# Kernel tuning notes

Hardware: AMD Instinct MI355X
Metric: run time of the kernel (lower is better)

The kernel has to match this reference:

```python
import jax, jax.numpy as jnp
import numpy as np

STATE_DIM = 32
CONTROL_DIM = 8
EMBED_DIM = 96
LATENT_DIM = STATE_DIM + EMBED_DIM  # 128
HIDDEN = 512
B, M = 2048, 64


def setup_inputs() -> dict:
    key = jax.random.key(0)
    ks = jax.random.split(key, 16)
    s = lambda k, shp, fan: jax.random.normal(k, shp, jnp.float32) * (1.0 / np.sqrt(fan))
    return {
        "x_k": jax.random.normal(ks[0], (B, STATE_DIM), jnp.float32),
        "u_seq": jax.random.normal(ks[1], (B, M, CONTROL_DIM), jnp.float32),
        "x_next_seq": jax.random.normal(ks[2], (B, M, STATE_DIM), jnp.float32),
        # encoder MLP (depth=3): in->h, h->h, h->h, h->embed
        "W1": s(ks[3], (STATE_DIM, HIDDEN), STATE_DIM), "b1": jnp.zeros((HIDDEN,), jnp.float32),
        "W2": s(ks[4], (HIDDEN, HIDDEN), HIDDEN), "b2": jnp.zeros((HIDDEN,), jnp.float32),
        "W3": s(ks[5], (HIDDEN, HIDDEN), HIDDEN), "b3": jnp.zeros((HIDDEN,), jnp.float32),
        "Wo": s(ks[6], (HIDDEN, EMBED_DIM), HIDDEN), "bo": jnp.zeros((EMBED_DIM,), jnp.float32),
        # Koopman operators (Linear, no bias); stored as [in, out]
        "A": s(ks[7], (LATENT_DIM, LATENT_DIM), LATENT_DIM),
        "Bmat": s(ks[8], (CONTROL_DIM, LATENT_DIM), CONTROL_DIM),
    }


def _encode(x, W1, b1, W2, b2, W3, b3, Wo, bo):
    h = jax.nn.relu(x @ W1 + b1)
    h = jax.nn.relu(h @ W2 + b2)
    h = jax.nn.relu(h @ W3 + b3)
    return h @ Wo + bo


def _lift(x, W1, b1, W2, b2, W3, b3, Wo, bo):
    return jnp.concatenate([x, _encode(x, W1, b1, W2, b2, W3, b3, Wo, bo)], axis=-1)


def reference(x_k, u_seq, x_next_seq, W1, b1, W2, b2, W3, b3, Wo, bo, A, Bmat):
    m = u_seq.shape[1]
    z_k = _lift(x_k, W1, b1, W2, b2, W3, b3, Wo, bo)  # [B, L]
    # lift targets (encoder applied to flattened [B*M, S])
    z_target_seq = _lift(x_next_seq.reshape(-1, STATE_DIM), W1, b1, W2, b2, W3, b3, Wo, bo)
    z_target_seq = z_target_seq.reshape(-1, m, LATENT_DIM)
    # precompute control contributions, then sequential LTI recurrence via scan
    bu = jnp.einsum('bmc,cl->mbl', u_seq, Bmat)  # [M, B, L]

    def step(z, bu_i):
        z_next = z @ A + bu_i
        return z_next, z_next

    _, z_pred = jax.lax.scan(step, z_k, bu)  # [M, B, L]
    z_pred_seq = jnp.transpose(z_pred, (1, 0, 2))  # [B, M, L]
    x_pred_seq = z_pred_seq[..., :STATE_DIM]
    return (z_pred_seq, x_pred_seq, z_target_seq)
```

## Files before the change

kernel.cpp:

```cpp
#include <hip/hip_runtime.h>


typedef unsigned short u16;
typedef __attribute__((ext_vector_type(8))) short bf16x8;
typedef __attribute__((ext_vector_type(4))) short bf16x4;
typedef __attribute__((ext_vector_type(4))) float f32x4;

#define OFF_W1 0
#define OFF_W2 16384
#define OFF_W3 278528
#define OFF_WO 540672
#define OFF_ZK_BYTES 1179648

#define XPRED_OFF 16777216
#define ZTGT_OFF  20971520

__device__ __forceinline__ float bf2f(u16 u) {
  unsigned int i = ((unsigned int)u) << 16;
  return __builtin_bit_cast(float, i);
}
__device__ __forceinline__ u16 f2bf(float f) {
  unsigned int i = __builtin_bit_cast(unsigned int, f);
  i = (i + 0x7FFFu + ((i >> 16) & 1u)) >> 16;
  return (u16)i;
}

__global__ void prep_swizzle(const float* __restrict__ W1, const float* __restrict__ W2,
                             const float* __restrict__ W3, const float* __restrict__ Wo,
                             u16* __restrict__ dst) {
  int f = blockIdx.x;
  int l = threadIdx.x;
  const float* src; int K, N; u16* d;
  if (f < 32)        { src = W1; K = 32;  N = 512; d = dst + OFF_W1; }
  else if (f < 544)  { src = W2; K = 512; N = 512; d = dst + OFF_W2; f -= 32; }
  else if (f < 1056) { src = W3; K = 512; N = 512; d = dst + OFF_W3; f -= 544; }
  else               { src = Wo; K = 512; N = 96;  d = dst + OFF_WO; f -= 1056; }
  const int KF = K >> 5;
  const int ct = f / KF, ks = f - ct * KF;
  const int q = l >> 4, n = l & 15;
  const int kbase = ks * 32 + q * 8;
  const int col = ct * 16 + n;
  bf16x8 vh;
  #pragma unroll
  for (int j = 0; j < 8; ++j)
    vh[j] = (short)f2bf(src[(size_t)(kbase + j) * N + col]);
  *(bf16x8*)(d + ((size_t)f * 64 + l) * 8) = vh;
}

__device__ __forceinline__ void store_h(const f32x4 (&acc)[4][4],
                                        const float* __restrict__ bias,
                                        u16* hbuf, int wv, int q, int n) {
  __syncthreads();
  #pragma unroll
  for (int i = 0; i < 4; ++i) {
    const int col = wv * 64 + i * 16 + n;
    const float bia = bias[col];
    #pragma unroll
    for (int rg = 0; rg < 4; ++rg) {
      #pragma unroll
      for (int r = 0; r < 4; ++r) {
        const int row = rg * 16 + q * 4 + r;
        hbuf[(row * 512 + col) ^ ((row & 7) << 3)] = f2bf(fmaxf(acc[rg][i][r] + bia, 0.f));
      }
    }
  }
  __syncthreads();
}

__device__ __forceinline__ void big_layer(const u16* __restrict__ wb,
                                          const float* __restrict__ bias,
                                          u16* hbuf, int wv, int l, int q, int n) {
  f32x4 acc[4][4];
  #pragma unroll
  for (int rg = 0; rg < 4; ++rg)
    #pragma unroll
    for (int i = 0; i < 4; ++i) acc[rg][i] = (f32x4){0.f, 0.f, 0.f, 0.f};
  #pragma unroll 2
  for (int ks = 0; ks < 16; ++ks) {
    bf16x8 b[4], a[4];
    #pragma unroll
    for (int i = 0; i < 4; ++i)
      b[i] = *(const bf16x8*)(wb + (size_t)((4 * wv + i) * 16 + ks) * 512 + (size_t)l * 8);
    #pragma unroll
    for (int rg = 0; rg < 4; ++rg) {
      const int row = rg * 16 + n;
      a[rg] = *(const bf16x8*)&hbuf[(row * 512 + ks * 32 + q * 8) ^ ((row & 7) << 3)];
    }
    #pragma unroll
    for (int rg = 0; rg < 4; ++rg)
      #pragma unroll
      for (int i = 0; i < 4; ++i)
        acc[rg][i] = __builtin_amdgcn_mfma_f32_16x16x32_bf16(a[rg], b[i], acc[rg][i], 0, 0, 0);
  }
  store_h(acc, bias, hbuf, wv, q, n);
}

__global__ __launch_bounds__(512, 2) void encoder_tgt(
    const float* __restrict__ xnext, const u16* __restrict__ wf,
    const float* __restrict__ b1, const float* __restrict__ b2,
    const float* __restrict__ b3, const float* __restrict__ bo_,
    float* __restrict__ ztgt) {
  __shared__ __align__(16) u16 hbuf[64 * 512];
  const int tid = threadIdx.x;
  const int wv = tid >> 6, l = tid & 63;
  const int q = l >> 4, n = l & 15;
  const size_t row0 = (size_t)blockIdx.x * 64;

  {
    const int r = tid >> 3, k0 = (tid & 7) * 4;
    f32x4 x = *(const f32x4*)(xnext + (row0 + r) * 32 + k0);
    *(f32x4*)(ztgt + (row0 + r) * 128 + k0) = x;
    bf16x4 v;
    #pragma unroll
    for (int j = 0; j < 4; ++j) v[j] = (short)f2bf(x[j]);
    *(bf16x4*)&hbuf[(r * 512 + k0) ^ ((r & 7) << 3)] = v;
  }
  __syncthreads();

  {
    f32x4 acc[4][4];
    #pragma unroll
    for (int rg = 0; rg < 4; ++rg)
      #pragma unroll
      for (int i = 0; i < 4; ++i) acc[rg][i] = (f32x4){0.f, 0.f, 0.f, 0.f};
    bf16x8 a[4];
    #pragma unroll
    for (int rg = 0; rg < 4; ++rg) {
      const int row = rg * 16 + n;
      a[rg] = *(const bf16x8*)&hbuf[(row * 512 + q * 8) ^ ((row & 7) << 3)];
    }
    #pragma unroll
    for (int i = 0; i < 4; ++i) {
      bf16x8 b = *(const bf16x8*)(wf + OFF_W1 + (size_t)(4 * wv + i) * 512 + (size_t)l * 8);
      #pragma unroll
      for (int rg = 0; rg < 4; ++rg)
        acc[rg][i] = __builtin_amdgcn_mfma_f32_16x16x32_bf16(a[rg], b, acc[rg][i], 0, 0, 0);
    }
    store_h(acc, b1, hbuf, wv, q, n);
  }

  big_layer(wf + OFF_W2, b2, hbuf, wv, l, q, n);
  big_layer(wf + OFF_W3, b3, hbuf, wv, l, q, n);

  if (wv < 6) {
    f32x4 o[4];
    #pragma unroll
    for (int rg = 0; rg < 4; ++rg) o[rg] = (f32x4){0.f, 0.f, 0.f, 0.f};
    #pragma unroll 2
    for (int ks = 0; ks < 16; ++ks) {
      bf16x8 b = *(const bf16x8*)(wf + OFF_WO + (size_t)(wv * 16 + ks) * 512 + (size_t)l * 8);
      #pragma unroll
      for (int rg = 0; rg < 4; ++rg) {
        const int row = rg * 16 + n;
        bf16x8 a = *(const bf16x8*)&hbuf[(row * 512 + ks * 32 + q * 8) ^ ((row & 7) << 3)];
        o[rg] = __builtin_amdgcn_mfma_f32_16x16x32_bf16(a, b, o[rg], 0, 0, 0);
      }
    }
    const float bia = bo_[wv * 16 + n];
    #pragma unroll
    for (int rg = 0; rg < 4; ++rg)
      #pragma unroll
      for (int r = 0; r < 4; ++r)
        ztgt[(row0 + rg * 16 + q * 4 + r) * 128 + 32 + wv * 16 + n] = o[rg][r] + bia;
  }
}

__global__ __launch_bounds__(256) void encoder_zk_f32(
    const float* __restrict__ xk,
    const float* __restrict__ W1, const float* __restrict__ b1,
    const float* __restrict__ W2, const float* __restrict__ b2,
    const float* __restrict__ W3, const float* __restrict__ b3,
    const float* __restrict__ Wo, const float* __restrict__ bo_,
    float* __restrict__ zk_out) {
  __shared__ __align__(16) float hb[2][8][512];
  __shared__ __align__(16) float xb[8][32];
  const int t = threadIdx.x;
  const int row0 = blockIdx.x * 8;
  {
    int r = t >> 5, j = t & 31;
    float v = xk[(size_t)(row0 + r) * 32 + j];
    xb[r][j] = v;
    zk_out[(size_t)(row0 + r) * 128 + j] = v;
  }
  __syncthreads();
  const int c0 = t, c1 = t + 256;
  {
    float a0[8], a1[8];
    const float i0 = b1[c0], i1 = b1[c1];
    #pragma unroll
    for (int r = 0; r < 8; ++r) { a0[r] = i0; a1[r] = i1; }
    for (int k = 0; k < 32; k += 4) {
      float w00 = W1[(size_t)(k+0)*512 + c0], w10 = W1[(size_t)(k+0)*512 + c1];
      float w01 = W1[(size_t)(k+1)*512 + c0], w11 = W1[(size_t)(k+1)*512 + c1];
      float w02 = W1[(size_t)(k+2)*512 + c0], w12 = W1[(size_t)(k+2)*512 + c1];
      float w03 = W1[(size_t)(k+3)*512 + c0], w13 = W1[(size_t)(k+3)*512 + c1];
      #pragma unroll
      for (int r = 0; r < 8; ++r) {
        f32x4 z = *(const f32x4*)&xb[r][k];
        a0[r] += z[0]*w00 + z[1]*w01 + z[2]*w02 + z[3]*w03;
        a1[r] += z[0]*w10 + z[1]*w11 + z[2]*w12 + z[3]*w13;
      }
    }
    #pragma unroll
    for (int r = 0; r < 8; ++r) { hb[0][r][c0] = fmaxf(a0[r], 0.f); hb[0][r][c1] = fmaxf(a1[r], 0.f); }
  }
  __syncthreads();
  #pragma unroll
  for (int lyr = 0; lyr < 2; ++lyr) {
    const float* W = lyr ? W3 : W2;
    const float* bb = lyr ? b3 : b2;
    const float (*hin)[512] = hb[lyr & 1];
    float (*hout)[512] = hb[(lyr & 1) ^ 1];
    float a0[8], a1[8];
    const float i0 = bb[c0], i1 = bb[c1];
    #pragma unroll
    for (int r = 0; r < 8; ++r) { a0[r] = i0; a1[r] = i1; }
    for (int k = 0; k < 512; k += 4) {
      float w00 = W[(size_t)(k+0)*512 + c0], w10 = W[(size_t)(k+0)*512 + c1];
      float w01 = W[(size_t)(k+1)*512 + c0], w11 = W[(size_t)(k+1)*512 + c1];
      float w02 = W[(size_t)(k+2)*512 + c0], w12 = W[(size_t)(k+2)*512 + c1];
      float w03 = W[(size_t)(k+3)*512 + c0], w13 = W[(size_t)(k+3)*512 + c1];
      #pragma unroll
      for (int r = 0; r < 8; ++r) {
        f32x4 z = *(const f32x4*)&hin[r][k];
        a0[r] += z[0]*w00 + z[1]*w01 + z[2]*w02 + z[3]*w03;
        a1[r] += z[0]*w10 + z[1]*w11 + z[2]*w12 + z[3]*w13;
      }
    }
    #pragma unroll
    for (int r = 0; r < 8; ++r) { hout[r][c0] = fmaxf(a0[r], 0.f); hout[r][c1] = fmaxf(a1[r], 0.f); }
    __syncthreads();
  }
  if (t < 96) {
    float a[8];
    const float i0 = bo_[t];
    #pragma unroll
    for (int r = 0; r < 8; ++r) a[r] = i0;
    for (int k = 0; k < 512; k += 4) {
      float w0 = Wo[(size_t)(k+0)*96 + t];
      float w1 = Wo[(size_t)(k+1)*96 + t];
      float w2 = Wo[(size_t)(k+2)*96 + t];
      float w3 = Wo[(size_t)(k+3)*96 + t];
      #pragma unroll
      for (int r = 0; r < 8; ++r) {
        f32x4 z = *(const f32x4*)&hb[0][r][k];
        a[r] += z[0]*w0 + z[1]*w1 + z[2]*w2 + z[3]*w3;
      }
    }
    #pragma unroll
    for (int r = 0; r < 8; ++r)
      zk_out[(size_t)(row0 + r) * 128 + 32 + t] = a[r];
  }
}

__global__ __launch_bounds__(256, 2) void scan_kernel(
    const float* __restrict__ zk, const float* __restrict__ Af,
    const float* __restrict__ Bm, const float* __restrict__ useq,
    float* __restrict__ zpred, float* __restrict__ xpred) {
  __shared__ __align__(16) float ubuf[4 * 512];
  __shared__ __align__(16) float zbuf[2][4 * 128];
  const int t = threadIdx.x;
  const int b0 = blockIdx.x * 4;
  const int c = t & 127, g = t >> 7;

  *(f32x4*)&ubuf[t * 4]        = *(const f32x4*)(useq + (size_t)b0 * 512 + t * 4);
  *(f32x4*)&ubuf[1024 + t * 4] = *(const f32x4*)(useq + (size_t)b0 * 512 + 1024 + t * 4);
  if (t < 128) *(f32x4*)&zbuf[0][t * 4] = *(const f32x4*)(zk + (size_t)b0 * 128 + t * 4);

  f32x4 ar[32];
  #pragma unroll
  for (int kk = 0; kk < 32; ++kk) {
    ar[kk][0] = Af[(size_t)(4 * kk + 0) * 128 + c];
    ar[kk][1] = Af[(size_t)(4 * kk + 1) * 128 + c];
    ar[kk][2] = Af[(size_t)(4 * kk + 2) * 128 + c];
    ar[kk][3] = Af[(size_t)(4 * kk + 3) * 128 + c];
  }
  float bm[8];
  #pragma unroll
  for (int j = 0; j < 8; ++j) bm[j] = Bm[j * 128 + c];
  __syncthreads();

  const int r0 = 2 * g, r1 = 2 * g + 1;
  const size_t o0 = (size_t)(b0 + r0) * 64;
  const size_t o1 = (size_t)(b0 + r1) * 64;
  int cur = 0;
  #pragma unroll 1
  for (int s = 0; s < 64; ++s) {
    f32x4 ua0 = *(const f32x4*)&ubuf[r0 * 512 + s * 8];
    f32x4 ub0 = *(const f32x4*)&ubuf[r0 * 512 + s * 8 + 4];
    f32x4 ua1 = *(const f32x4*)&ubuf[r1 * 512 + s * 8];
    f32x4 ub1 = *(const f32x4*)&ubuf[r1 * 512 + s * 8 + 4];
    f32x4 v0, v1;
    #pragma unroll
    for (int j = 0; j < 4; ++j) {
      v0[j] = ua0[j] * bm[j] + ub0[j] * bm[4 + j];
      v1[j] = ua1[j] * bm[j] + ub1[j] * bm[4 + j];
    }
    const float* z0p = &zbuf[cur][r0 * 128];
    const float* z1p = &zbuf[cur][r1 * 128];
    #pragma unroll
    for (int kk = 0; kk < 32; ++kk) {
      f32x4 a  = ar[kk];
      f32x4 za = *(const f32x4*)&z0p[kk * 4];
      f32x4 zb = *(const f32x4*)&z1p[kk * 4];
      v0 += za * a;
      v1 += zb * a;
    }
    const float acc0 = (v0[0] + v0[1]) + (v0[2] + v0[3]);
    const float acc1 = (v1[0] + v1[1]) + (v1[2] + v1[3]);
    zbuf[cur ^ 1][r0 * 128 + c] = acc0;
    zbuf[cur ^ 1][r1 * 128 + c] = acc1;
    zpred[(o0 + s) * 128 + c] = acc0;
    zpred[(o1 + s) * 128 + c] = acc1;
    if (c < 32) {
      xpred[(o0 + s) * 32 + c] = acc0;
      xpred[(o1 + s) * 32 + c] = acc1;
    }
    __syncthreads();
    cur ^= 1;
  }
}

extern "C" void kernel_launch(void* const* d_in, const int* in_sizes, int n_in,
                              void* d_out, int out_size, void* d_ws, size_t ws_size,
                              hipStream_t stream) {
  (void)in_sizes; (void)n_in; (void)out_size; (void)ws_size;
  const float* xk    = (const float*)d_in[0];
  const float* useq  = (const float*)d_in[1];
  const float* xnext = (const float*)d_in[2];
  const float* W1 = (const float*)d_in[3];
  const float* b1 = (const float*)d_in[4];
  const float* W2 = (const float*)d_in[5];
  const float* b2 = (const float*)d_in[6];
  const float* W3 = (const float*)d_in[7];
  const float* b3 = (const float*)d_in[8];
  const float* Wo = (const float*)d_in[9];
  const float* bo = (const float*)d_in[10];
  const float* A  = (const float*)d_in[11];
  const float* Bm = (const float*)d_in[12];

  float* out   = (float*)d_out;
  float* zpred = out;
  float* xpred = out + XPRED_OFF;
  float* ztgt  = out + ZTGT_OFF;
  u16*   wf    = (u16*)d_ws;
  float* zkw   = (float*)((char*)d_ws + OFF_ZK_BYTES);

  prep_swizzle<<<1152, 64, 0, stream>>>(W1, W2, W3, Wo, wf);
  encoder_zk_f32<<<256, 256, 0, stream>>>(xk, W1, b1, W2, b2, W3, b3, Wo, bo, zkw);
  scan_kernel<<<512, 256, 0, stream>>>(zkw, A, Bm, useq, zpred, xpred);
  encoder_tgt<<<2048, 512, 0, stream>>>(xnext, wf, b1, b2, b3, bo, ztgt);
}
```

Baseline: 528.7 us.

## Move Koopman scan to split-bf16 MFMA and widen encoder blocks

The scan recurrence now runs on bf16 MFMA with a hi/lo split of both A and z (three MFMAs per tile) to approximate fp32 accuracy. A is pre-split by the prep kernel and loaded into LDS with global_load_lds, and each block handles 8 batch rows instead of 4. The target encoder moves to 1024-thread blocks covering 128 rows, uses packed bf16 conversion on store, and the zk encoder uses 512 threads with one column each. The split-bf16 product can lose some precision against fp32, and the larger LDS footprint may lower occupancy.

```diff
diff --git a/kernel.cpp b/kernel.cpp
--- a/kernel.cpp
+++ b/kernel.cpp
@@ -11,6 +11,8 @@
 #define OFF_W3 278528
 #define OFF_WO 540672
 #define OFF_ZK_BYTES 1179648
+#define OFF_AH 1114112
+#define OFF_AL 1130496
 
 #define XPRED_OFF 16777216
 #define ZTGT_OFF  20971520
@@ -27,14 +29,16 @@
 
 __global__ void prep_swizzle(const float* __restrict__ W1, const float* __restrict__ W2,
                              const float* __restrict__ W3, const float* __restrict__ Wo,
-                             u16* __restrict__ dst) {
+                             const float* __restrict__ Am, u16* __restrict__ dst) {
   int f = blockIdx.x;
   int l = threadIdx.x;
-  const float* src; int K, N; u16* d;
+  const float* src; int K, N; u16* d; int lo = 0;
   if (f < 32)        { src = W1; K = 32;  N = 512; d = dst + OFF_W1; }
   else if (f < 544)  { src = W2; K = 512; N = 512; d = dst + OFF_W2; f -= 32; }
   else if (f < 1056) { src = W3; K = 512; N = 512; d = dst + OFF_W3; f -= 544; }
-  else               { src = Wo; K = 512; N = 96;  d = dst + OFF_WO; f -= 1056; }
+  else if (f < 1152) { src = Wo; K = 512; N = 96;  d = dst + OFF_WO; f -= 1056; }
+  else if (f < 1184) { src = Am; K = 128; N = 128; d = dst + OFF_AH; f -= 1152; }
+  else               { src = Am; K = 128; N = 128; d = dst + OFF_AL; f -= 1184; lo = 1; }
   const int KF = K >> 5;
   const int ct = f / KF, ks = f - ct * KF;
   const int q = l >> 4, n = l & 15;
@@ -42,26 +46,37 @@
   const int col = ct * 16 + n;
   bf16x8 vh;
   #pragma unroll
-  for (int j = 0; j < 8; ++j)
-    vh[j] = (short)f2bf(src[(size_t)(kbase + j) * N + col]);
+  for (int j = 0; j < 8; ++j) {
+    float v = src[(size_t)(kbase + j) * N + col];
+    u16 h = f2bf(v);
+    if (lo) h = f2bf(v - bf2f(h));
+    vh[j] = (short)h;
+  }
   *(bf16x8*)(d + ((size_t)f * 64 + l) * 8) = vh;
 }
 
 __device__ __forceinline__ void store_h(const f32x4 (&acc)[4][4],
                                         const float* __restrict__ bias,
-                                        u16* hbuf, int wv, int q, int n) {
+                                        u16* hbuf, int rh, int cg, int q, int n) {
   __syncthreads();
   #pragma unroll
   for (int i = 0; i < 4; ++i) {
-    const int col = wv * 64 + i * 16 + n;
+    const int col = cg * 64 + i * 16 + n;
     const float bia = bias[col];
     #pragma unroll
     for (int rg = 0; rg < 4; ++rg) {
-      #pragma unroll
-      for (int r = 0; r < 4; ++r) {
-        const int row = rg * 16 + q * 4 + r;
-        hbuf[(row * 512 + col) ^ ((row & 7) << 3)] = f2bf(fmaxf(acc[rg][i][r] + bia, 0.f));
-      }
+      const int rb = rh * 64 + rg * 16 + q * 4;
+      float f0 = fmaxf(acc[rg][i][0] + bia, 0.f);
+      float f1 = fmaxf(acc[rg][i][1] + bia, 0.f);
+      float f2 = fmaxf(acc[rg][i][2] + bia, 0.f);
+      float f3 = fmaxf(acc[rg][i][3] + bia, 0.f);
+      unsigned p01, p23;
+      asm("v_cvt_pk_bf16_f32 %0, %1, %2" : "=v"(p01) : "v"(f0), "v"(f1));
+      asm("v_cvt_pk_bf16_f32 %0, %1, %2" : "=v"(p23) : "v"(f2), "v"(f3));
+      hbuf[((rb + 0) * 512 + col) ^ (((rb + 0) & 7) << 3)] = (u16)(p01 & 0xFFFFu);
+      hbuf[((rb + 1) * 512 + col) ^ (((rb + 1) & 7) << 3)] = (u16)(p01 >> 16);
+      hbuf[((rb + 2) * 512 + col) ^ (((rb + 2) & 7) << 3)] = (u16)(p23 & 0xFFFFu);
+      hbuf[((rb + 3) * 512 + col) ^ (((rb + 3) & 7) << 3)] = (u16)(p23 >> 16);
     }
   }
   __syncthreads();
@@ -69,7 +84,7 @@
 
 __device__ __forceinline__ void big_layer(const u16* __restrict__ wb,
                                           const float* __restrict__ bias,
-                                          u16* hbuf, int wv, int l, int q, int n) {
+                                          u16* hbuf, int rh, int cg, int l, int q, int n) {
   f32x4 acc[4][4];
   #pragma unroll
   for (int rg = 0; rg < 4; ++rg)
@@ -80,10 +95,10 @@
     bf16x8 b[4], a[4];
     #pragma unroll
     for (int i = 0; i < 4; ++i)
-      b[i] = *(const bf16x8*)(wb + (size_t)((4 * wv + i) * 16 + ks) * 512 + (size_t)l * 8);
+      b[i] = *(const bf16x8*)(wb + (size_t)((4 * cg + i) * 16 + ks) * 512 + (size_t)l * 8);
     #pragma unroll
     for (int rg = 0; rg < 4; ++rg) {
-      const int row = rg * 16 + n;
+      const int row = rh * 64 + rg * 16 + n;
       a[rg] = *(const bf16x8*)&hbuf[(row * 512 + ks * 32 + q * 8) ^ ((row & 7) << 3)];
     }
     #pragma unroll
@@ -92,19 +107,20 @@
       for (int i = 0; i < 4; ++i)
         acc[rg][i] = __builtin_amdgcn_mfma_f32_16x16x32_bf16(a[rg], b[i], acc[rg][i], 0, 0, 0);
   }
-  store_h(acc, bias, hbuf, wv, q, n);
-}
-
-__global__ __launch_bounds__(512, 2) void encoder_tgt(
+  store_h(acc, bias, hbuf, rh, cg, q, n);
+}
+
+__global__ __launch_bounds__(1024, 4) void encoder_tgt(
     const float* __restrict__ xnext, const u16* __restrict__ wf,
     const float* __restrict__ b1, const float* __restrict__ b2,
     const float* __restrict__ b3, const float* __restrict__ bo_,
     float* __restrict__ ztgt) {
-  __shared__ __align__(16) u16 hbuf[64 * 512];
+  __shared__ __align__(16) u16 hbuf[128 * 512];
   const int tid = threadIdx.x;
   const int wv = tid >> 6, l = tid & 63;
   const int q = l >> 4, n = l & 15;
-  const size_t row0 = (size_t)blockIdx.x * 64;
+  const int rh = wv >> 3, cg = wv & 7;
+  const size_t row0 = (size_t)blockIdx.x * 128;
 
   {
     const int r = tid >> 3, k0 = (tid & 7) * 4;
@@ -126,46 +142,46 @@
     bf16x8 a[4];
     #pragma unroll
     for (int rg = 0; rg < 4; ++rg) {
-      const int row = rg * 16 + n;
+      const int row = rh * 64 + rg * 16 + n;
       a[rg] = *(const bf16x8*)&hbuf[(row * 512 + q * 8) ^ ((row & 7) << 3)];
     }
     #pragma unroll
     for (int i = 0; i < 4; ++i) {
-      bf16x8 b = *(const bf16x8*)(wf + OFF_W1 + (size_t)(4 * wv + i) * 512 + (size_t)l * 8);
+      bf16x8 b = *(const bf16x8*)(wf + OFF_W1 + (size_t)(4 * cg + i) * 512 + (size_t)l * 8);
       #pragma unroll
       for (int rg = 0; rg < 4; ++rg)
         acc[rg][i] = __builtin_amdgcn_mfma_f32_16x16x32_bf16(a[rg], b, acc[rg][i], 0, 0, 0);
     }
-    store_h(acc, b1, hbuf, wv, q, n);
-  }
-
-  big_layer(wf + OFF_W2, b2, hbuf, wv, l, q, n);
-  big_layer(wf + OFF_W3, b3, hbuf, wv, l, q, n);
-
-  if (wv < 6) {
+    store_h(acc, b1, hbuf, rh, cg, q, n);
+  }
+
+  big_layer(wf + OFF_W2, b2, hbuf, rh, cg, l, q, n);
+  big_layer(wf + OFF_W3, b3, hbuf, rh, cg, l, q, n);
+
+  if (cg < 6) {
     f32x4 o[4];
     #pragma unroll
     for (int rg = 0; rg < 4; ++rg) o[rg] = (f32x4){0.f, 0.f, 0.f, 0.f};
     #pragma unroll 2
     for (int ks = 0; ks < 16; ++ks) {
-      bf16x8 b = *(const bf16x8*)(wf + OFF_WO + (size_t)(wv * 16 + ks) * 512 + (size_t)l * 8);
+      bf16x8 b = *(const bf16x8*)(wf + OFF_WO + (size_t)(cg * 16 + ks) * 512 + (size_t)l * 8);
       #pragma unroll
       for (int rg = 0; rg < 4; ++rg) {
-        const int row = rg * 16 + n;
+        const int row = rh * 64 + rg * 16 + n;
         bf16x8 a = *(const bf16x8*)&hbuf[(row * 512 + ks * 32 + q * 8) ^ ((row & 7) << 3)];
         o[rg] = __builtin_amdgcn_mfma_f32_16x16x32_bf16(a, b, o[rg], 0, 0, 0);
       }
     }
-    const float bia = bo_[wv * 16 + n];
+    const float bia = bo_[cg * 16 + n];
     #pragma unroll
     for (int rg = 0; rg < 4; ++rg)
       #pragma unroll
       for (int r = 0; r < 4; ++r)
-        ztgt[(row0 + rg * 16 + q * 4 + r) * 128 + 32 + wv * 16 + n] = o[rg][r] + bia;
-  }
-}
-
-__global__ __launch_bounds__(256) void encoder_zk_f32(
+        ztgt[(row0 + rh * 64 + rg * 16 + q * 4 + r) * 128 + 32 + cg * 16 + n] = o[rg][r] + bia;
+  }
+}
+
+__global__ __launch_bounds__(512) void encoder_zk_f32(
     const float* __restrict__ xk,
     const float* __restrict__ W1, const float* __restrict__ b1,
     const float* __restrict__ W2, const float* __restrict__ b2,
@@ -176,33 +192,32 @@
   __shared__ __align__(16) float xb[8][32];
   const int t = threadIdx.x;
   const int row0 = blockIdx.x * 8;
-  {
+  if (t < 256) {
     int r = t >> 5, j = t & 31;
     float v = xk[(size_t)(row0 + r) * 32 + j];
     xb[r][j] = v;
     zk_out[(size_t)(row0 + r) * 128 + j] = v;
   }
   __syncthreads();
-  const int c0 = t, c1 = t + 256;
+  const int c = t;
   {
-    float a0[8], a1[8];
-    const float i0 = b1[c0], i1 = b1[c1];
-    #pragma unroll
-    for (int r = 0; r < 8; ++r) { a0[r] = i0; a1[r] = i1; }
+    float a[8];
+    const float i0 = b1[c];
+    #pragma unroll
+    for (int r = 0; r < 8; ++r) a[r] = i0;
     for (int k = 0; k < 32; k += 4) {
-      float w00 = W1[(size_t)(k+0)*512 + c0], w10 = W1[(size_t)(k+0)*512 + c1];
-      float w01 = W1[(size_t)(k+1)*512 + c0], w11 = W1[(size_t)(k+1)*512 + c1];
-      float w02 = W1[(size_t)(k+2)*512 + c0], w12 = W1[(size_t)(k+2)*512 + c1];
-      float w03 = W1[(size_t)(k+3)*512 + c0], w13 = W1[(size_t)(k+3)*512 + c1];
+      float w0 = W1[(size_t)(k+0)*512 + c];
+      float w1 = W1[(size_t)(k+1)*512 + c];
+      float w2 = W1[(size_t)(k+2)*512 + c];
+      float w3 = W1[(size_t)(k+3)*512 + c];
       #pragma unroll
       for (int r = 0; r < 8; ++r) {
         f32x4 z = *(const f32x4*)&xb[r][k];
-        a0[r] += z[0]*w00 + z[1]*w01 + z[2]*w02 + z[3]*w03;
-        a1[r] += z[0]*w10 + z[1]*w11 + z[2]*w12 + z[3]*w13;
-      }
-    }
-    #pragma unroll
-    for (int r = 0; r < 8; ++r) { hb[0][r][c0] = fmaxf(a0[r], 0.f); hb[0][r][c1] = fmaxf(a1[r], 0.f); }
+        a[r] += z[0]*w0 + z[1]*w1 + z[2]*w2 + z[3]*w3;
+      }
+    }
+    #pragma unroll
+    for (int r = 0; r < 8; ++r) hb[0][r][c] = fmaxf(a[r], 0.f);
   }
   __syncthreads();
   #pragma unroll
@@ -211,24 +226,23 @@
     const float* bb = lyr ? b3 : b2;
     const float (*hin)[512] = hb[lyr & 1];
     float (*hout)[512] = hb[(lyr & 1) ^ 1];
-    float a0[8], a1[8];
-    const float i0 = bb[c0], i1 = bb[c1];
-    #pragma unroll
-    for (int r = 0; r < 8; ++r) { a0[r] = i0; a1[r] = i1; }
+    float a[8];
+    const float i0 = bb[c];
+    #pragma unroll
+    for (int r = 0; r < 8; ++r) a[r] = i0;
     for (int k = 0; k < 512; k += 4) {
-      float w00 = W[(size_t)(k+0)*512 + c0], w10 = W[(size_t)(k+0)*512 + c1];
-      float w01 = W[(size_t)(k+1)*512 + c0], w11 = W[(size_t)(k+1)*512 + c1];
-      float w02 = W[(size_t)(k+2)*512 + c0], w12 = W[(size_t)(k+2)*512 + c1];
-      float w03 = W[(size_t)(k+3)*512 + c0], w13 = W[(size_t)(k+3)*512 + c1];
+      float w0 = W[(size_t)(k+0)*512 + c];
+      float w1 = W[(size_t)(k+1)*512 + c];
+      float w2 = W[(size_t)(k+2)*512 + c];
+      float w3 = W[(size_t)(k+3)*512 + c];
       #pragma unroll
       for (int r = 0; r < 8; ++r) {
         f32x4 z = *(const f32x4*)&hin[r][k];
-        a0[r] += z[0]*w00 + z[1]*w01 + z[2]*w02 + z[3]*w03;
-        a1[r] += z[0]*w10 + z[1]*w11 + z[2]*w12 + z[3]*w13;
-      }
-    }
-    #pragma unroll
-    for (int r = 0; r < 8; ++r) { hout[r][c0] = fmaxf(a0[r], 0.f); hout[r][c1] = fmaxf(a1[r], 0.f); }
+        a[r] += z[0]*w0 + z[1]*w1 + z[2]*w2 + z[3]*w3;
+      }
+    }
+    #pragma unroll
+    for (int r = 0; r < 8; ++r) hout[r][c] = fmaxf(a[r], 0.f);
     __syncthreads();
   }
   if (t < 96) {
@@ -253,71 +267,104 @@
   }
 }
 
-__global__ __launch_bounds__(256, 2) void scan_kernel(
-    const float* __restrict__ zk, const float* __restrict__ Af,
+__global__ __launch_bounds__(256) void scan_mfma(
+    const float* __restrict__ zk, const u16* __restrict__ wf,
     const float* __restrict__ Bm, const float* __restrict__ useq,
     float* __restrict__ zpred, float* __restrict__ xpred) {
-  __shared__ __align__(16) float ubuf[4 * 512];
-  __shared__ __align__(16) float zbuf[2][4 * 128];
+  __shared__ __align__(16) u16 ahf[32 * 512];
+  __shared__ __align__(16) u16 alf[32 * 512];
+  __shared__ __align__(16) float ubuf[8 * 512];
+  __shared__ __align__(16) float zbuf[8][132];
+  __shared__ __align__(16) u16 zh[16][136];
+  __shared__ __align__(16) u16 zl[16][136];
+  __shared__ __align__(16) float bu[8][132];
   const int t = threadIdx.x;
-  const int b0 = blockIdx.x * 4;
-  const int c = t & 127, g = t >> 7;
-
-  *(f32x4*)&ubuf[t * 4]        = *(const f32x4*)(useq + (size_t)b0 * 512 + t * 4);
-  *(f32x4*)&ubuf[1024 + t * 4] = *(const f32x4*)(useq + (size_t)b0 * 512 + 1024 + t * 4);
-  if (t < 128) *(f32x4*)&zbuf[0][t * 4] = *(const f32x4*)(zk + (size_t)b0 * 128 + t * 4);
-
-  f32x4 ar[32];
-  #pragma unroll
-  for (int kk = 0; kk < 32; ++kk) {
-    ar[kk][0] = Af[(size_t)(4 * kk + 0) * 128 + c];
-    ar[kk][1] = Af[(size_t)(4 * kk + 1) * 128 + c];
-    ar[kk][2] = Af[(size_t)(4 * kk + 2) * 128 + c];
-    ar[kk][3] = Af[(size_t)(4 * kk + 3) * 128 + c];
-  }
-  float bm[8];
-  #pragma unroll
-  for (int j = 0; j < 8; ++j) bm[j] = Bm[j * 128 + c];
-  __syncthreads();
-
-  const int r0 = 2 * g, r1 = 2 * g + 1;
-  const size_t o0 = (size_t)(b0 + r0) * 64;
-  const size_t o1 = (size_t)(b0 + r1) * 64;
-  int cur = 0;
-  #pragma unroll 1
+  const int wv = t >> 6, l = t & 63;
+  const int q = l >> 4, n = l & 15;
+  const size_t b0 = (size_t)blockIdx.x * 8;
+
+  #pragma unroll
+  for (int i = 0; i < 8; ++i) {
+    const int f = wv * 8 + i;
+    __builtin_amdgcn_global_load_lds(
+        (const __attribute__((address_space(1))) unsigned int*)(wf + OFF_AH + (size_t)f * 512 + l * 8),
+        (__attribute__((address_space(3))) unsigned int*)(ahf + (size_t)f * 512), 16, 0, 0);
+    __builtin_amdgcn_global_load_lds(
+        (const __attribute__((address_space(1))) unsigned int*)(wf + OFF_AL + (size_t)f * 512 + l * 8),
+        (__attribute__((address_space(3))) unsigned int*)(alf + (size_t)f * 512), 16, 0, 0);
+  }
+  {
+    const float* us = useq + b0 * 512;
+    #pragma unroll
+    for (int i = 0; i < 4; ++i)
+      *(f32x4*)&ubuf[i * 1024 + t * 4] = *(const f32x4*)(us + i * 1024 + t * 4);
+  }
+  const int crow = t >> 5, cc0 = (t & 31) * 4;
+  *(f32x4*)&zbuf[crow][cc0] = *(const f32x4*)(zk + (b0 + crow) * 128 + cc0);
+  for (int i = t; i < 8 * 136; i += 256) { (&zh[8][0])[i] = 0; (&zl[8][0])[i] = 0; }
+  f32x4 bmr[8];
+  #pragma unroll
+  for (int j = 0; j < 8; ++j) bmr[j] = *(const f32x4*)(Bm + (size_t)j * 128 + cc0);
+  __syncthreads();
+
+  const int ct0 = 2 * wv, ct1 = 2 * wv + 1;
   for (int s = 0; s < 64; ++s) {
-    f32x4 ua0 = *(const f32x4*)&ubuf[r0 * 512 + s * 8];
-    f32x4 ub0 = *(const f32x4*)&ubuf[r0 * 512 + s * 8 + 4];
-    f32x4 ua1 = *(const f32x4*)&ubuf[r1 * 512 + s * 8];
-    f32x4 ub1 = *(const f32x4*)&ubuf[r1 * 512 + s * 8 + 4];
-    f32x4 v0, v1;
-    #pragma unroll
-    for (int j = 0; j < 4; ++j) {
-      v0[j] = ua0[j] * bm[j] + ub0[j] * bm[4 + j];
-      v1[j] = ua1[j] * bm[j] + ub1[j] * bm[4 + j];
-    }
-    const float* z0p = &zbuf[cur][r0 * 128];
-    const float* z1p = &zbuf[cur][r1 * 128];
-    #pragma unroll
-    for (int kk = 0; kk < 32; ++kk) {
-      f32x4 a  = ar[kk];
-      f32x4 za = *(const f32x4*)&z0p[kk * 4];
-      f32x4 zb = *(const f32x4*)&z1p[kk * 4];
-      v0 += za * a;
-      v1 += zb * a;
-    }
-    const float acc0 = (v0[0] + v0[1]) + (v0[2] + v0[3]);
-    const float acc1 = (v1[0] + v1[1]) + (v1[2] + v1[3]);
-    zbuf[cur ^ 1][r0 * 128 + c] = acc0;
-    zbuf[cur ^ 1][r1 * 128 + c] = acc1;
-    zpred[(o0 + s) * 128 + c] = acc0;
-    zpred[(o1 + s) * 128 + c] = acc1;
-    if (c < 32) {
-      xpred[(o0 + s) * 32 + c] = acc0;
-      xpred[(o1 + s) * 32 + c] = acc1;
+    {
+      f32x4 z = *(const f32x4*)&zbuf[crow][cc0];
+      bf16x4 vh, vl;
+      #pragma unroll
+      for (int i = 0; i < 4; ++i) {
+        u16 h = f2bf(z[i]);
+        vh[i] = (short)h;
+        vl[i] = (short)f2bf(z[i] - bf2f(h));
+      }
+      *(bf16x4*)&zh[crow][cc0] = vh;
+      *(bf16x4*)&zl[crow][cc0] = vl;
+      f32x4 uu0 = *(const f32x4*)&ubuf[crow * 512 + s * 8];
+      f32x4 uu1 = *(const f32x4*)&ubuf[crow * 512 + s * 8 + 4];
+      f32x4 bv = uu0[0] * bmr[0];
+      bv += uu0[1] * bmr[1]; bv += uu0[2] * bmr[2]; bv += uu0[3] * bmr[3];
+      bv += uu1[0] * bmr[4]; bv += uu1[1] * bmr[5]; bv += uu1[2] * bmr[6]; bv += uu1[3] * bmr[7];
+      *(f32x4*)&bu[crow][cc0] = bv;
     }
     __syncthreads();
-    cur ^= 1;
+    f32x4 acc0 = {0.f, 0.f, 0.f, 0.f};
+    f32x4 acc1 = {0.f, 0.f, 0.f, 0.f};
+    #pragma unroll
+    for (int ks = 0; ks < 4; ++ks) {
+      const int ko = ks * 32 + q * 8;
+      bf16x8 azh = *(const bf16x8*)&zh[n][ko];
+      bf16x8 azl = *(const bf16x8*)&zl[n][ko];
+      bf16x8 bh0 = *(const bf16x8*)&ahf[(size_t)(ct0 * 4 + ks) * 512 + l * 8];
+      bf16x8 bl0 = *(const bf16x8*)&alf[(size_t)(ct0 * 4 + ks) * 512 + l * 8];
+      bf16x8 bh1 = *(const bf16x8*)&ahf[(size_t)(ct1 * 4 + ks) * 512 + l * 8];
+      bf16x8 bl1 = *(const bf16x8*)&alf[(size_t)(ct1 * 4 + ks) * 512 + l * 8];
+      acc0 = __builtin_amdgcn_mfma_f32_16x16x32_bf16(azh, bh0, acc0, 0, 0, 0);
+      acc0 = __builtin_amdgcn_mfma_f32_16x16x32_bf16(azl, bh0, acc0, 0, 0, 0);
+      acc0 = __builtin_amdgcn_mfma_f32_16x16x32_bf16(azh, bl0, acc0, 0, 0, 0);
+      acc1 = __builtin_amdgcn_mfma_f32_16x16x32_bf16(azh, bh1, acc1, 0, 0, 0);
+      acc1 = __builtin_amdgcn_mfma_f32_16x16x32_bf16(azl, bh1, acc1, 0, 0, 0);
+      acc1 = __builtin_amdgcn_mfma_f32_16x16x32_bf16(azh, bl1, acc1, 0, 0, 0);
+    }
+    if (q < 2) {
+      #pragma unroll
+      for (int r = 0; r < 4; ++r) {
+        const int row = q * 4 + r;
+        const int c0 = ct0 * 16 + n, c1 = ct1 * 16 + n;
+        const float v0 = acc0[r] + bu[row][c0];
+        const float v1 = acc1[r] + bu[row][c1];
+        zbuf[row][c0] = v0;
+        zbuf[row][c1] = v1;
+        const size_t go = (b0 + row) * 64 + s;
+        zpred[go * 128 + c0] = v0;
+        zpred[go * 128 + c1] = v1;
+        if (wv == 0) {
+          xpred[go * 32 + c0] = v0;
+          xpred[go * 32 + c1] = v1;
+        }
+      }
+    }
+    __syncthreads();
   }
 }
 
@@ -346,8 +393,8 @@
   u16*   wf    = (u16*)d_ws;
   float* zkw   = (float*)((char*)d_ws + OFF_ZK_BYTES);
 
-  prep_swizzle<<<1152, 64, 0, stream>>>(W1, W2, W3, Wo, wf);
-  encoder_zk_f32<<<256, 256, 0, stream>>>(xk, W1, b1, W2, b2, W3, b3, Wo, bo, zkw);
-  scan_kernel<<<512, 256, 0, stream>>>(zkw, A, Bm, useq, zpred, xpred);
-  encoder_tgt<<<2048, 512, 0, stream>>>(xnext, wf, b1, b2, b3, bo, ztgt);
-}
+  prep_swizzle<<<1216, 64, 0, stream>>>(W1, W2, W3, Wo, A, wf);
+  encoder_zk_f32<<<256, 512, 0, stream>>>(xk, W1, b1, W2, b2, W3, b3, Wo, bo, zkw);
+  scan_mfma<<<256, 256, 0, stream>>>(zkw, wf, Bm, useq, zpred, xpred);
+  encoder_tgt<<<1024, 1024, 0, stream>>>(xnext, wf, b1, b2, b3, bo, ztgt);
+}
```

Measured after the change: 561.7 us. +6.3%, slower.
